# Kernel tuning notes

Hardware: AMD Instinct MI355X
Metric: run time of the kernel (lower is better)

Reference implementation:

```python
import jax, jax.numpy as jnp
import numpy as np

B, T, E = 2, 2048, 1024
H = 16
DH = E // H  # 64
DFF = 4 * E
EPS = 1e-5


def _layernorm(x, gamma, beta):
    mu = jnp.mean(x, axis=-1, keepdims=True)
    var = jnp.mean((x - mu) ** 2, axis=-1, keepdims=True)
    return (x - mu) * jax.lax.rsqrt(var + EPS) * gamma + beta


def setup_inputs() -> dict:
    key = jax.random.key(0)
    ks = jax.random.split(key, 16)
    s_e = 1.0 / np.sqrt(E)
    s_f = 1.0 / np.sqrt(DFF)
    return {
        "x": jax.random.normal(ks[0], (B, T, E), jnp.float32),
        # per-head QKV projections, stacked over heads [H, E, DH]
        "Wq": jax.random.normal(ks[1], (H, E, DH), jnp.float32) * s_e,
        "bq": jnp.zeros((H, DH), jnp.float32),
        "Wk": jax.random.normal(ks[2], (H, E, DH), jnp.float32) * s_e,
        "bk": jnp.zeros((H, DH), jnp.float32),
        "Wv": jax.random.normal(ks[3], (H, E, DH), jnp.float32) * s_e,
        "bv": jnp.zeros((H, DH), jnp.float32),
        # output projection
        "Wo": jax.random.normal(ks[4], (E, E), jnp.float32) * s_e,
        "bo": jnp.zeros((E,), jnp.float32),
        # feed-forward
        "W1": jax.random.normal(ks[5], (E, DFF), jnp.float32) * s_e,
        "b1": jnp.zeros((DFF,), jnp.float32),
        "W2": jax.random.normal(ks[6], (DFF, E), jnp.float32) * s_f,
        "b2": jnp.zeros((E,), jnp.float32),
        # layernorms
        "gamma1": jnp.ones((E,), jnp.float32),
        "beta1": jnp.zeros((E,), jnp.float32),
        "gamma2": jnp.ones((E,), jnp.float32),
        "beta2": jnp.zeros((E,), jnp.float32),
    }


def reference(x, Wq, bq, Wk, bk, Wv, bv, Wo, bo, W1, b1, W2, b2,
              gamma1, beta1, gamma2, beta2):
    Bc, Tc, Ec = x.shape
    # --- multi-head causal self-attention (dropout = eval/identity) ---
    xn = _layernorm(x, gamma1, beta1)
    q = jnp.einsum('bte,hed->bhtd', xn, Wq) + bq[:, None, :]
    k = jnp.einsum('bte,hed->bhtd', xn, Wk) + bk[:, None, :]
    v = jnp.einsum('bte,hed->bhtd', xn, Wv) + bv[:, None, :]
    scale = 1.0 / np.sqrt(q.shape[-1])
    scores = jnp.einsum('bhtd,bhsd->bhts', q, k) * scale  # [B,H,T,T]
    causal = jnp.tril(jnp.ones((Tc, Tc), bool))
    scores = jnp.where(causal, scores, jnp.float32(-1e9))
    attn = jax.nn.softmax(scores, axis=-1)
    out = jnp.einsum('bhts,bhsd->bhtd', attn, v)          # [B,H,T,DH]
    out = out.transpose(0, 2, 1, 3).reshape(Bc, Tc, Ec)    # concat heads
    out = out @ Wo + bo
    x = x + out
    # --- feed-forward ---
    xn2 = _layernorm(x, gamma2, beta2)
    h = jax.nn.relu(xn2 @ W1 + b1)
    x = x + (h @ W2 + b2)
    return x
```

## Files before the change

kernel.cpp:

```cpp
#include <hip/hip_runtime.h>
#include <stdint.h>

#define BT    4096
#define EDIM  1024
#define TLEN  2048
#define NH    16
#define DHH   64
#define DFFN  4096

typedef short short8 __attribute__((ext_vector_type(8)));
typedef float f32x4  __attribute__((ext_vector_type(4)));

typedef const __attribute__((address_space(1))) unsigned int* gas_ptr;
typedef __attribute__((address_space(3))) unsigned int*       las_ptr;

__device__ __forceinline__ float bf2f(unsigned short u) {
    union { unsigned int i; float f; } c; c.i = ((unsigned int)u) << 16; return c.f;
}
__device__ __forceinline__ unsigned short f2bf(float f) {
    union { float f; unsigned int i; } c; c.f = f;
    unsigned int u = c.i;
    unsigned int r = u + 0x7fffu + ((u >> 16) & 1u);
    return (unsigned short)(r >> 16);
}
__device__ __forceinline__ unsigned short f2bf_trunc(float f) {
    union { float f; unsigned int i; } c; c.f = f;
    return (unsigned short)(c.i >> 16);
}
__device__ __forceinline__ float fexp2(float x) {
#if __has_builtin(__builtin_amdgcn_exp2f)
    return __builtin_amdgcn_exp2f(x);
#else
    return __expf(x * 0.69314718056f);
#endif
}
__device__ __forceinline__ void gload16(const unsigned short* g, unsigned short* l) {
    __builtin_amdgcn_global_load_lds((gas_ptr)g, (las_ptr)l, 16, 0, 0);
}

template<int QKV>
__global__ __launch_bounds__(256) void transpose_kernel(
    const float* src, unsigned short* dst, int Kdim, int srcStride)
{
    __shared__ float T[64][65];
    int t = threadIdx.x;
    int n0 = blockIdx.x * 64, k0 = blockIdx.y * 64;
    int r = t >> 4, c4 = (t & 15) * 4;
    #pragma unroll
    for (int i = 0; i < 4; i++) {
        int rr = r + i * 16;
        const float* p;
        if (QKV) p = src + ((size_t)(n0 >> 6)) * 65536 + (size_t)(k0 + rr) * 64 + c4;
        else     p = src + (size_t)(k0 + rr) * srcStride + n0 + c4;
        float4 v = *(const float4*)p;
        T[c4 + 0][rr] = v.x;
        T[c4 + 1][rr] = v.y;
        T[c4 + 2][rr] = v.z;
        T[c4 + 3][rr] = v.w;
    }
    __syncthreads();
    int rn = t >> 2, ck = (t & 3) * 16;
    short8 o0, o1;
    #pragma unroll
    for (int j = 0; j < 8; j++) o0[j] = (short)f2bf(T[rn][ck + j]);
    #pragma unroll
    for (int j = 0; j < 8; j++) o1[j] = (short)f2bf(T[rn][ck + 8 + j]);
    unsigned short* dp = dst + (size_t)(n0 + rn) * Kdim + k0 + ck;
    *(short8*)dp       = o0;
    *(short8*)(dp + 8) = o1;
}

__global__ __launch_bounds__(256) void transpose_qkv3_kernel(
    const float* __restrict__ Wq, const float* __restrict__ Wk,
    const float* __restrict__ Wv, unsigned short* __restrict__ dstbase)
{
    __shared__ float T[64][65];
    int z = blockIdx.z;
    const float* src = (z == 0) ? Wq : (z == 1) ? Wk : Wv;
    unsigned short* dst = dstbase + (size_t)z * 1048576;
    int t = threadIdx.x;
    int n0 = blockIdx.x * 64, k0 = blockIdx.y * 64;
    int r = t >> 4, c4 = (t & 15) * 4;
    #pragma unroll
    for (int i = 0; i < 4; i++) {
        int rr = r + i * 16;
        const float* p = src + ((size_t)(n0 >> 6)) * 65536 + (size_t)(k0 + rr) * 64 + c4;
        float4 v = *(const float4*)p;
        T[c4 + 0][rr] = v.x;
        T[c4 + 1][rr] = v.y;
        T[c4 + 2][rr] = v.z;
        T[c4 + 3][rr] = v.w;
    }
    __syncthreads();
    int rn = t >> 2, ck = (t & 3) * 16;
    short8 o0, o1;
    #pragma unroll
    for (int j = 0; j < 8; j++) o0[j] = (short)f2bf(T[rn][ck + j]);
    #pragma unroll
    for (int j = 0; j < 8; j++) o1[j] = (short)f2bf(T[rn][ck + 8 + j]);
    unsigned short* dp = dst + (size_t)(n0 + rn) * EDIM + k0 + ck;
    *(short8*)dp       = o0;
    *(short8*)(dp + 8) = o1;
}

__global__ __launch_bounds__(256) void vtrans_kernel(
    const unsigned short* __restrict__ v, unsigned short* __restrict__ vt)
{
    __shared__ __align__(16) unsigned short T[64][72];
    int bh = blockIdx.x, st = blockIdx.y;
    int t = threadIdx.x;
    int r = t >> 2, c = (t & 3) * 16;
    const unsigned short* src = v + ((size_t)bh * TLEN + st * 64) * DHH;
    short8 a0 = *(const short8*)(src + r * DHH + c);
    short8 a1 = *(const short8*)(src + r * DHH + c + 8);
    *(short8*)&T[r][c]     = a0;
    *(short8*)&T[r][c + 8] = a1;
    __syncthreads();
    int d = t >> 2;
    short8 o0, o1;
    #pragma unroll
    for (int j = 0; j < 8; j++) o0[j] = (short)T[c + j][d];
    #pragma unroll
    for (int j = 0; j < 8; j++) o1[j] = (short)T[c + 8 + j][d];
    unsigned short* dst = vt + ((size_t)bh * DHH + d) * TLEN + st * 64 + c;
    *(short8*)dst       = o0;
    *(short8*)(dst + 8) = o1;
}

__global__ __launch_bounds__(256) void bias_fuse_kernel(
    const float* __restrict__ bq, const float* __restrict__ bk,
    const float* __restrict__ bv, float* __restrict__ dst)
{
    int t = blockIdx.x * 256 + threadIdx.x;
    const float* src = (t < 1024) ? bq : (t < 2048) ? bk : bv;
    dst[t] = src[t & 1023];
}

template<int F32IN>
__global__ __launch_bounds__(256) void ln_fused_kernel(
    const void* __restrict__ x, const float* __restrict__ g,
    const float* __restrict__ b, unsigned short* __restrict__ out)
{
    int row = blockIdx.x, tid = threadIdx.x;
    size_t off = (size_t)row * EDIM + tid * 4;
    float v0, v1, v2, v3;
    if (F32IN) {
        float4 a = *(const float4*)((const float*)x + off);
        v0 = a.x; v1 = a.y; v2 = a.z; v3 = a.w;
    } else {
        ushort4 raw = *(const ushort4*)((const unsigned short*)x + off);
        v0 = bf2f(raw.x); v1 = bf2f(raw.y); v2 = bf2f(raw.z); v3 = bf2f(raw.w);
    }
    float s  = v0 + v1 + v2 + v3;
    float ss = v0*v0 + v1*v1 + v2*v2 + v3*v3;
    #pragma unroll
    for (int o = 1; o < 64; o <<= 1) {
        s  += __shfl_xor(s,  o, 64);
        ss += __shfl_xor(ss, o, 64);
    }
    __shared__ float red[8];
    int wave = tid >> 6;
    if ((tid & 63) == 0) { red[wave*2] = s; red[wave*2+1] = ss; }
    __syncthreads();
    s  = red[0] + red[2] + red[4] + red[6];
    ss = red[1] + red[3] + red[5] + red[7];
    float m  = s * (1.0f / EDIM);
    float rs = rsqrtf(ss * (1.0f / EDIM) - m * m + 1e-5f);
    float4 gv = *(const float4*)(g + tid * 4);
    float4 bv = *(const float4*)(b + tid * 4);
    ushort4 o;
    o.x = f2bf((v0 - m) * rs * gv.x + bv.x);
    o.y = f2bf((v1 - m) * rs * gv.y + bv.y);
    o.z = f2bf((v2 - m) * rs * gv.z + bv.z);
    o.w = f2bf((v3 - m) * rs * gv.w + bv.w);
    *(ushort4*)(out + off) = o;
}

#define V_QKV  0
#define V_WO   1
#define V_FF1  2
#define V_FF2A 3
#define V_FF2B 4

template<int VARIANT, int BN>
__global__ __launch_bounds__(256) void gemm_bt_kernel(
    const unsigned short* A,
    const unsigned short* Bt,
    const float* bias,
    const void* resid,
    void* out,
    int N, int K)
{
    constexpr int NJ = BN / 32;
    __shared__ __align__(16) unsigned short As[128 * 64];
    __shared__ __align__(16) unsigned short Bs[BN * 64];
    int tid  = threadIdx.x;
    int lane = tid & 63, wave = tid >> 6;
    int quad = lane >> 4, l16 = lane & 15;
    int wr = wave >> 1, wc = wave & 1;
    int m0 = blockIdx.y * 128, n0 = blockIdx.x * BN;

    f32x4 acc[4][NJ];
    #pragma unroll
    for (int i = 0; i < 4; i++)
        #pragma unroll
        for (int j = 0; j < NJ; j++) acc[i][j] = (f32x4){0.f, 0.f, 0.f, 0.f};

    int lr = lane >> 3;
    int lc = (lane & 7) * 8;

    for (int k0 = 0; k0 < K; k0 += 64) {
        #pragma unroll
        for (int i = 0; i < 4; i++) {
            int r = (i * 4 + wave) * 8 + lr;
            gload16(A + (size_t)(m0 + r) * K + k0 + lc, &As[(i * 4 + wave) * 512]);
        }
        #pragma unroll
        for (int i = 0; i < NJ; i++) {
            int r = (i * 4 + wave) * 8 + lr;
            gload16(Bt + (size_t)(n0 + r) * K + k0 + lc, &Bs[(i * 4 + wave) * 512]);
        }
        __syncthreads();

        #pragma unroll
        for (int ks = 0; ks < 2; ks++) {
            short8 af[4], bf[NJ];
            #pragma unroll
            for (int i = 0; i < 4; i++)
                af[i] = *(const short8*)(&As[(wr * 64 + i * 16 + l16) * 64 + ks * 32 + quad * 8]);
            #pragma unroll
            for (int j = 0; j < NJ; j++)
                bf[j] = *(const short8*)(&Bs[(wc * (BN / 2) + j * 16 + l16) * 64 + ks * 32 + quad * 8]);
            #pragma unroll
            for (int i = 0; i < 4; i++)
                #pragma unroll
                for (int j = 0; j < NJ; j++)
                    acc[i][j] = __builtin_amdgcn_mfma_f32_16x16x32_bf16(af[i], bf[j], acc[i][j], 0, 0, 0);
        }

        __syncthreads();
    }

    #pragma unroll
    for (int j = 0; j < NJ; j++) {
        int c = n0 + wc * (BN / 2) + j * 16 + l16;
        float bi = (VARIANT == V_FF2A) ? 0.0f : bias[c];
        #pragma unroll
        for (int i = 0; i < 4; i++) {
            #pragma unroll
            for (int r = 0; r < 4; r++) {
                int m = m0 + wr * 64 + i * 16 + quad * 4 + r;
                float val = acc[i][j][r] + bi;
                if (VARIANT == V_WO)
                    val += ((const float*)resid)[(size_t)m * N + c];
                if (VARIANT == V_FF2B)
                    val += bf2f(((const unsigned short*)resid)[(size_t)m * N + c])
                         + ((const float*)out)[(size_t)m * N + c];
                if (VARIANT == V_FF1)
                    val = fmaxf(val, 0.0f);
                if (VARIANT == V_QKV) {
                    int b = m >> 11, t = m & 2047;
                    int mat = c >> 10, cc = c & 1023;
                    int h = cc >> 6, d = cc & 63;
                    ((unsigned short*)out)[(size_t)mat * 4194304 +
                        (((size_t)(b * NH + h)) * TLEN + t) * DHH + d] = f2bf(val);
                } else if (VARIANT == V_FF2A || VARIANT == V_FF2B) {
                    ((float*)out)[(size_t)m * N + c] = val;
                } else {
                    ((unsigned short*)out)[(size_t)m * N + c] = f2bf(val);
                }
            }
        }
    }
}

__global__ __launch_bounds__(256) void attn_kernel(
    const unsigned short* __restrict__ q,
    const unsigned short* __restrict__ k,
    const unsigned short* __restrict__ vt,
    unsigned short* __restrict__ att)
{
    __shared__ __align__(16) unsigned short Ks[128 * 72];
    __shared__ __align__(16) unsigned short Vs[64 * 136];
    __shared__ __align__(16) unsigned short Ps[4][16 * 136];
    int tid  = threadIdx.x;
    int lane = tid & 63, wave = tid >> 6;
    int quad = lane >> 4, l16 = lane & 15;

    int flat = blockIdx.x;
    int xcd  = flat & 7, idx = flat >> 3;
    int bh   = xcd * 4 + (idx >> 5);
    int qt   = 31 - (idx & 31);
    int q0   = qt * 64;
    int qw   = q0 + wave * 16;

    const unsigned short* Qb = q  + ((size_t)bh * TLEN + qw) * DHH;
    const unsigned short* Kb = k  + (size_t)bh * TLEN * DHH;
    const unsigned short* Vb = vt + (size_t)bh * DHH * TLEN;

    short8 aq0 = *(const short8*)(Qb + l16 * DHH + quad * 8);
    short8 aq1 = *(const short8*)(Qb + l16 * DHH + 32 + quad * 8);

    f32x4 o[4];
    #pragma unroll
    for (int n = 0; n < 4; n++) o[n] = (f32x4){0.f, 0.f, 0.f, 0.f};
    f32x4 mrow = {-1e30f, -1e30f, -1e30f, -1e30f};
    f32x4 lrow = {0.f, 0.f, 0.f, 0.f};
    unsigned short* Pw = Ps[wave];
    const float cs = 0.18033688011f;

    int rowK = tid >> 1, colK = (tid & 1) * 32;
    int rowV = tid >> 2, colV = (tid & 3) * 32;

    int nch = (q0 >> 7) + 1;

    short8 ka0, ka1, ka2, ka3, va0, va1, va2, va3;
    {
        const unsigned short* kp = Kb + (size_t)rowK * DHH + colK;
        ka0 = *(const short8*)kp;
        ka1 = *(const short8*)(kp + 8);
        ka2 = *(const short8*)(kp + 16);
        ka3 = *(const short8*)(kp + 24);
        const unsigned short* vp = Vb + (size_t)rowV * TLEN + colV;
        va0 = *(const short8*)vp;
        va1 = *(const short8*)(vp + 8);
        va2 = *(const short8*)(vp + 16);
        va3 = *(const short8*)(vp + 24);
    }

    for (int ch = 0; ch < nch; ch++) {
        int s0 = ch * 128;
        __syncthreads();
        *(short8*)(&Ks[rowK * 72 + colK])       = ka0;
        *(short8*)(&Ks[rowK * 72 + colK + 8])   = ka1;
        *(short8*)(&Ks[rowK * 72 + colK + 16])  = ka2;
        *(short8*)(&Ks[rowK * 72 + colK + 24])  = ka3;
        *(short8*)(&Vs[rowV * 136 + colV])      = va0;
        *(short8*)(&Vs[rowV * 136 + colV + 8])  = va1;
        *(short8*)(&Vs[rowV * 136 + colV + 16]) = va2;
        *(short8*)(&Vs[rowV * 136 + colV + 24]) = va3;
        __syncthreads();

        if (ch + 1 < nch) {
            int s1 = s0 + 128;
            const unsigned short* kp = Kb + (size_t)(s1 + rowK) * DHH + colK;
            ka0 = *(const short8*)kp;
            ka1 = *(const short8*)(kp + 8);
            ka2 = *(const short8*)(kp + 16);
            ka3 = *(const short8*)(kp + 24);
            const unsigned short* vp = Vb + (size_t)rowV * TLEN + s1 + colV;
            va0 = *(const short8*)vp;
            va1 = *(const short8*)(vp + 8);
            va2 = *(const short8*)(vp + 16);
            va3 = *(const short8*)(vp + 24);
        }

        f32x4 S[8];
        #pragma unroll
        for (int n = 0; n < 8; n++) {
            short8 b0 = *(const short8*)(&Ks[(n * 16 + l16) * 72 + quad * 8]);
            short8 b1 = *(const short8*)(&Ks[(n * 16 + l16) * 72 + 32 + quad * 8]);
            f32x4 s = (f32x4){0.f, 0.f, 0.f, 0.f};
            s = __builtin_amdgcn_mfma_f32_16x16x32_bf16(aq0, b0, s, 0, 0, 0);
            s = __builtin_amdgcn_mfma_f32_16x16x32_bf16(aq1, b1, s, 0, 0, 0);
            S[n] = s;
        }
        bool needmask = (s0 + 127 > qw);
        #pragma unroll
        for (int r = 0; r < 4; r++) {
            float xv[8];
            #pragma unroll
            for (int n = 0; n < 8; n++) {
                float xx = S[n][r] * cs;
                if (needmask && (s0 + n * 16 + l16 > qw + quad * 4 + r)) xx = -1e30f;
                xv[n] = xx;
            }
            float mxl = fmaxf(fmaxf(fmaxf(xv[0], xv[1]), fmaxf(xv[2], xv[3])),
                              fmaxf(fmaxf(xv[4], xv[5]), fmaxf(xv[6], xv[7])));
            float used;
            if (__all(mxl <= mrow[r] + 8.0f)) {
                used = mrow[r];
            } else {
                float mx = mxl;
                mx = fmaxf(mx, __shfl_xor(mx, 1, 64));
                mx = fmaxf(mx, __shfl_xor(mx, 2, 64));
                mx = fmaxf(mx, __shfl_xor(mx, 4, 64));
                mx = fmaxf(mx, __shfl_xor(mx, 8, 64));
                float mnew  = fmaxf(mrow[r], mx);
                float alpha = fexp2(mrow[r] - mnew);
                lrow[r] *= alpha;
                o[0][r] *= alpha; o[1][r] *= alpha;
                o[2][r] *= alpha; o[3][r] *= alpha;
                mrow[r] = mnew;
                used = mnew;
            }
            float ps = 0.f;
            int prow = (quad * 4 + r) * 136;
            #pragma unroll
            for (int n = 0; n < 8; n++) {
                float p = fexp2(xv[n] - used);
                ps += p;
                Pw[prow + n * 16 + l16] = f2bf_trunc(p);
            }
            lrow[r] += ps;
        }
        short8 ap[4];
        #pragma unroll
        for (int ks = 0; ks < 4; ks++)
            ap[ks] = *(const short8*)(Pw + l16 * 136 + ks * 32 + quad * 8);
        #pragma unroll
        for (int n = 0; n < 4; n++) {
            #pragma unroll
            for (int ks = 0; ks < 4; ks++) {
                short8 b = *(const short8*)(&Vs[(n * 16 + l16) * 136 + ks * 32 + quad * 8]);
                o[n] = __builtin_amdgcn_mfma_f32_16x16x32_bf16(ap[ks], b, o[n], 0, 0, 0);
            }
        }
    }

    int bidx = bh >> 4, hh = bh & 15;
    #pragma unroll
    for (int r = 0; r < 4; r++) {
        float ls = lrow[r];
        ls += __shfl_xor(ls, 1, 64);
        ls += __shfl_xor(ls, 2, 64);
        ls += __shfl_xor(ls, 4, 64);
        ls += __shfl_xor(ls, 8, 64);
        float inv = 1.0f / ls;
        int t = qw + quad * 4 + r;
        size_t rowoff = ((size_t)(bidx * TLEN + t)) * EDIM + hh * 64;
        #pragma unroll
        for (int n = 0; n < 4; n++)
            att[rowoff + n * 16 + l16] = f2bf(o[n][r] * inv);
    }
}

extern "C" void kernel_launch(void* const* d_in, const int* in_sizes, int n_in,
                              void* d_out, int out_size, void* d_ws, size_t ws_size,
                              hipStream_t stream)
{
    (void)in_sizes; (void)n_in; (void)out_size; (void)ws_size;
    const float* x   = (const float*)d_in[0];
    const float* Wq  = (const float*)d_in[1];
    const float* bq  = (const float*)d_in[2];
    const float* Wk  = (const float*)d_in[3];
    const float* bk  = (const float*)d_in[4];
    const float* Wv  = (const float*)d_in[5];
    const float* bv  = (const float*)d_in[6];
    const float* Wo  = (const float*)d_in[7];
    const float* bo  = (const float*)d_in[8];
    const float* W1  = (const float*)d_in[9];
    const float* b1  = (const float*)d_in[10];
    const float* W2  = (const float*)d_in[11];
    const float* b2  = (const float*)d_in[12];
    const float* g1  = (const float*)d_in[13];
    const float* be1 = (const float*)d_in[14];
    const float* g2  = (const float*)d_in[15];
    const float* be2 = (const float*)d_in[16];

    unsigned short* ws  = (unsigned short*)d_ws;
    unsigned short* xn  = ws;
    unsigned short* vtg = ws;
    unsigned short* qb  = ws + 4194304;
    unsigned short* kb  = ws + 8388608;
    unsigned short* vb  = ws + 12582912;
    unsigned short* wqt = ws + 16777216;
    unsigned short* att = ws + 16777216;
    unsigned short* x1  = ws + 4194304;
    unsigned short* wot = ws + 8388608;
    unsigned short* w1t = ws + 8388608;
    unsigned short* w2t = ws + 10485760;
    unsigned short* hb  = ws + 12582912;
    float* biasf = (float*)(ws + 19922944);

    dim3 gT64(16, 16);
    dim3 gE(EDIM / 64, BT / 128);
    dim3 gQKV(3072 / 128, BT / 128);
    dim3 gF(2048 / 128, BT / 128);

    transpose_qkv3_kernel<<<dim3(16, 16, 3), 256, 0, stream>>>(Wq, Wk, Wv, wqt);
    bias_fuse_kernel<<<dim3(12), 256, 0, stream>>>(bq, bk, bv, biasf);

    ln_fused_kernel<1><<<BT, 256, 0, stream>>>(x, g1, be1, xn);

    gemm_bt_kernel<V_QKV, 128><<<gQKV, 256, 0, stream>>>(xn, wqt, biasf, nullptr, qb, 3072, EDIM);

    vtrans_kernel<<<dim3(NH * 2, TLEN / 64), 256, 0, stream>>>(vb, vtg);

    attn_kernel<<<dim3(1024), 256, 0, stream>>>(qb, kb, vtg, att);

    transpose_kernel<0><<<gT64, 256, 0, stream>>>(Wo, wot, EDIM, EDIM);
    gemm_bt_kernel<V_WO, 64><<<gE, 256, 0, stream>>>(att, wot, bo, x, x1, EDIM, EDIM);

    ln_fused_kernel<0><<<BT, 256, 0, stream>>>(x1, g2, be2, xn);

    transpose_kernel<0><<<dim3(32, 16), 256, 0, stream>>>(W1, w1t, EDIM, DFFN);
    transpose_kernel<0><<<dim3(16, 32), 256, 0, stream>>>(W2, w2t, 2048, EDIM);
    gemm_bt_kernel<V_FF1, 128><<<gF, 256, 0, stream>>>(xn, w1t, b1, nullptr, hb, 2048, EDIM);
    gemm_bt_kernel<V_FF2A, 64><<<gE, 256, 0, stream>>>(hb, w2t, nullptr, nullptr, d_out, EDIM, 2048);
    transpose_kernel<0><<<dim3(32, 16), 256, 0, stream>>>(W1 + 2048, w1t, EDIM, DFFN);
    transpose_kernel<0><<<dim3(16, 32), 256, 0, stream>>>(W2 + (size_t)2048 * EDIM, w2t, 2048, EDIM);
    gemm_bt_kernel<V_FF1, 128><<<gF, 256, 0, stream>>>(xn, w1t, b1 + 2048, nullptr, hb, 2048, EDIM);
    gemm_bt_kernel<V_FF2B, 64><<<gE, 256, 0, stream>>>(hb, w2t, b2, x1, d_out, EDIM, 2048);
}
```

Before: 442.5 us.

## Process two query tiles per attention block, swizzle GEMM grid, fuse FFN transposes

The attention kernel now handles 128 query rows per block, with each wave processing two 16-row groups, so every K/V chunk loaded into shared memory serves twice as many queries and the block count halves. The GEMMs switch to a 1D grid with an XCD-aware remap of block index to tile, intended to improve L2 locality across the chiplets. The paired W1/W2 transpose launches are merged into a single kernel using blockIdx.z, which cuts launch count. Costs are higher register pressure in attention and fewer blocks, which may worsen causal load imbalance.

```diff
diff --git a/kernel.cpp b/kernel.cpp
--- a/kernel.cpp
+++ b/kernel.cpp
@@ -99,6 +99,43 @@
     #pragma unroll
     for (int j = 0; j < 8; j++) o1[j] = (short)f2bf(T[rn][ck + 8 + j]);
     unsigned short* dp = dst + (size_t)(n0 + rn) * EDIM + k0 + ck;
+    *(short8*)dp       = o0;
+    *(short8*)(dp + 8) = o1;
+}
+
+__global__ __launch_bounds__(256) void transpose_ffn_kernel(
+    const float* __restrict__ W1h, const float* __restrict__ W2h,
+    unsigned short* __restrict__ w1t, unsigned short* __restrict__ w2t)
+{
+    __shared__ float T[64][65];
+    int z = blockIdx.z;
+    const float* src;
+    unsigned short* dst;
+    int Kdim, sstride, n0, k0;
+    if (z == 0) { src = W1h; dst = w1t; Kdim = 1024; sstride = 4096;
+                  n0 = blockIdx.x * 64; k0 = blockIdx.y * 64; }
+    else        { src = W2h; dst = w2t; Kdim = 2048; sstride = 1024;
+                  n0 = blockIdx.y * 64; k0 = blockIdx.x * 64; }
+    int t = threadIdx.x;
+    int r = t >> 4, c4 = (t & 15) * 4;
+    #pragma unroll
+    for (int i = 0; i < 4; i++) {
+        int rr = r + i * 16;
+        const float* p = src + (size_t)(k0 + rr) * sstride + n0 + c4;
+        float4 v = *(const float4*)p;
+        T[c4 + 0][rr] = v.x;
+        T[c4 + 1][rr] = v.y;
+        T[c4 + 2][rr] = v.z;
+        T[c4 + 3][rr] = v.w;
+    }
+    __syncthreads();
+    int rn = t >> 2, ck = (t & 3) * 16;
+    short8 o0, o1;
+    #pragma unroll
+    for (int j = 0; j < 8; j++) o0[j] = (short)f2bf(T[rn][ck + j]);
+    #pragma unroll
+    for (int j = 0; j < 8; j++) o1[j] = (short)f2bf(T[rn][ck + 8 + j]);
+    unsigned short* dp = dst + (size_t)(n0 + rn) * Kdim + k0 + ck;
     *(short8*)dp       = o0;
     *(short8*)(dp + 8) = o1;
 }
@@ -189,7 +226,7 @@
     const float* bias,
     const void* resid,
     void* out,
-    int N, int K)
+    int N, int K, int gx)
 {
     constexpr int NJ = BN / 32;
     __shared__ __align__(16) unsigned short As[128 * 64];
@@ -198,7 +235,11 @@
     int lane = tid & 63, wave = tid >> 6;
     int quad = lane >> 4, l16 = lane & 15;
     int wr = wave >> 1, wc = wave & 1;
-    int m0 = blockIdx.y * 128, n0 = blockIdx.x * BN;
+
+    int cpx  = (int)gridDim.x >> 3;
+    int flat = blockIdx.x;
+    int wg   = (flat & 7) * cpx + (flat >> 3);
+    int m0 = (wg / gx) * 128, n0 = (wg % gx) * BN;
 
     f32x4 acc[4][NJ];
     #pragma unroll
@@ -274,6 +315,76 @@
     }
 }
 
+__device__ __forceinline__ void attn_qh_pass(
+    const short8& aqa, const short8& aqb,
+    const unsigned short* Ks, const unsigned short* Vs, unsigned short* Pw,
+    f32x4* o, f32x4& mrow, f32x4& lrow,
+    int s0, int qw, int quad, int l16)
+{
+    const float cs = 0.18033688011f;
+    f32x4 S[8];
+    #pragma unroll
+    for (int n = 0; n < 8; n++) {
+        short8 b0 = *(const short8*)(&Ks[(n * 16 + l16) * 72 + quad * 8]);
+        short8 b1 = *(const short8*)(&Ks[(n * 16 + l16) * 72 + 32 + quad * 8]);
+        f32x4 s = (f32x4){0.f, 0.f, 0.f, 0.f};
+        s = __builtin_amdgcn_mfma_f32_16x16x32_bf16(aqa, b0, s, 0, 0, 0);
+        s = __builtin_amdgcn_mfma_f32_16x16x32_bf16(aqb, b1, s, 0, 0, 0);
+        S[n] = s;
+    }
+    bool needmask = (s0 + 127 > qw);
+    #pragma unroll
+    for (int r = 0; r < 4; r++) {
+        float xv[8];
+        #pragma unroll
+        for (int n = 0; n < 8; n++) {
+            float xx = S[n][r] * cs;
+            if (needmask && (s0 + n * 16 + l16 > qw + quad * 4 + r)) xx = -1e30f;
+            xv[n] = xx;
+        }
+        float mxl = fmaxf(fmaxf(fmaxf(xv[0], xv[1]), fmaxf(xv[2], xv[3])),
+                          fmaxf(fmaxf(xv[4], xv[5]), fmaxf(xv[6], xv[7])));
+        float used;
+        if (__all(mxl <= mrow[r] + 8.0f)) {
+            used = mrow[r];
+        } else {
+            float mx = mxl;
+            mx = fmaxf(mx, __shfl_xor(mx, 1, 64));
+            mx = fmaxf(mx, __shfl_xor(mx, 2, 64));
+            mx = fmaxf(mx, __shfl_xor(mx, 4, 64));
+            mx = fmaxf(mx, __shfl_xor(mx, 8, 64));
+            float mnew  = fmaxf(mrow[r], mx);
+            float alpha = fexp2(mrow[r] - mnew);
+            lrow[r] *= alpha;
+            o[0][r] *= alpha; o[1][r] *= alpha;
+            o[2][r] *= alpha; o[3][r] *= alpha;
+            mrow[r] = mnew;
+            used = mnew;
+        }
+        float ps = 0.f;
+        int prow = (quad * 4 + r) * 136;
+        #pragma unroll
+        for (int n = 0; n < 8; n++) {
+            float p = fexp2(xv[n] - used);
+            ps += p;
+            Pw[prow + n * 16 + l16] = f2bf_trunc(p);
+        }
+        lrow[r] += ps;
+    }
+    short8 ap[4];
+    #pragma unroll
+    for (int ks = 0; ks < 4; ks++)
+        ap[ks] = *(const short8*)(Pw + l16 * 136 + ks * 32 + quad * 8);
+    #pragma unroll
+    for (int n = 0; n < 4; n++) {
+        #pragma unroll
+        for (int ks = 0; ks < 4; ks++) {
+            short8 b = *(const short8*)(&Vs[(n * 16 + l16) * 136 + ks * 32 + quad * 8]);
+            o[n] = __builtin_amdgcn_mfma_f32_16x16x32_bf16(ap[ks], b, o[n], 0, 0, 0);
+        }
+    }
+}
+
 __global__ __launch_bounds__(256) void attn_kernel(
     const unsigned short* __restrict__ q,
     const unsigned short* __restrict__ k,
@@ -289,30 +400,36 @@
 
     int flat = blockIdx.x;
     int xcd  = flat & 7, idx = flat >> 3;
-    int bh   = xcd * 4 + (idx >> 5);
-    int qt   = 31 - (idx & 31);
-    int q0   = qt * 64;
-    int qw   = q0 + wave * 16;
-
-    const unsigned short* Qb = q  + ((size_t)bh * TLEN + qw) * DHH;
+    int bh   = xcd * 4 + (idx >> 4);
+    int qt   = 15 - (idx & 15);
+    int q0   = qt * 128;
+    int qw0  = q0 + wave * 16;
+    int qw1  = qw0 + 64;
+
     const unsigned short* Kb = k  + (size_t)bh * TLEN * DHH;
     const unsigned short* Vb = vt + (size_t)bh * DHH * TLEN;
-
-    short8 aq0 = *(const short8*)(Qb + l16 * DHH + quad * 8);
-    short8 aq1 = *(const short8*)(Qb + l16 * DHH + 32 + quad * 8);
-
-    f32x4 o[4];
-    #pragma unroll
-    for (int n = 0; n < 4; n++) o[n] = (f32x4){0.f, 0.f, 0.f, 0.f};
-    f32x4 mrow = {-1e30f, -1e30f, -1e30f, -1e30f};
-    f32x4 lrow = {0.f, 0.f, 0.f, 0.f};
+    const unsigned short* Q0 = q + ((size_t)bh * TLEN + qw0) * DHH;
+    const unsigned short* Q1 = q + ((size_t)bh * TLEN + qw1) * DHH;
+
+    short8 aq00 = *(const short8*)(Q0 + l16 * DHH + quad * 8);
+    short8 aq01 = *(const short8*)(Q0 + l16 * DHH + 32 + quad * 8);
+    short8 aq10 = *(const short8*)(Q1 + l16 * DHH + quad * 8);
+    short8 aq11 = *(const short8*)(Q1 + l16 * DHH + 32 + quad * 8);
+
+    f32x4 o0[4], o1[4];
+    #pragma unroll
+    for (int n = 0; n < 4; n++) {
+        o0[n] = (f32x4){0.f, 0.f, 0.f, 0.f};
+        o1[n] = (f32x4){0.f, 0.f, 0.f, 0.f};
+    }
+    f32x4 mrow0 = {-1e30f, -1e30f, -1e30f, -1e30f}, mrow1 = mrow0;
+    f32x4 lrow0 = {0.f, 0.f, 0.f, 0.f},            lrow1 = lrow0;
     unsigned short* Pw = Ps[wave];
-    const float cs = 0.18033688011f;
 
     int rowK = tid >> 1, colK = (tid & 1) * 32;
     int rowV = tid >> 2, colV = (tid & 3) * 32;
 
-    int nch = (q0 >> 7) + 1;
+    int nch = qt + 1;
 
     short8 ka0, ka1, ka2, ka3, va0, va1, va2, va3;
     {
@@ -355,83 +472,38 @@
             va3 = *(const short8*)(vp + 24);
         }
 
-        f32x4 S[8];
-        #pragma unroll
-        for (int n = 0; n < 8; n++) {
-            short8 b0 = *(const short8*)(&Ks[(n * 16 + l16) * 72 + quad * 8]);
-            short8 b1 = *(const short8*)(&Ks[(n * 16 + l16) * 72 + 32 + quad * 8]);
-            f32x4 s = (f32x4){0.f, 0.f, 0.f, 0.f};
-            s = __builtin_amdgcn_mfma_f32_16x16x32_bf16(aq0, b0, s, 0, 0, 0);
-            s = __builtin_amdgcn_mfma_f32_16x16x32_bf16(aq1, b1, s, 0, 0, 0);
-            S[n] = s;
-        }
-        bool needmask = (s0 + 127 > qw);
-        #pragma unroll
-        for (int r = 0; r < 4; r++) {
-            float xv[8];
-            #pragma unroll
-            for (int n = 0; n < 8; n++) {
-                float xx = S[n][r] * cs;
-                if (needmask && (s0 + n * 16 + l16 > qw + quad * 4 + r)) xx = -1e30f;
-                xv[n] = xx;
-            }
-            float mxl = fmaxf(fmaxf(fmaxf(xv[0], xv[1]), fmaxf(xv[2], xv[3])),
-                              fmaxf(fmaxf(xv[4], xv[5]), fmaxf(xv[6], xv[7])));
-            float used;
-            if (__all(mxl <= mrow[r] + 8.0f)) {
-                used = mrow[r];
-            } else {
-                float mx = mxl;
-                mx = fmaxf(mx, __shfl_xor(mx, 1, 64));
-                mx = fmaxf(mx, __shfl_xor(mx, 2, 64));
-                mx = fmaxf(mx, __shfl_xor(mx, 4, 64));
-                mx = fmaxf(mx, __shfl_xor(mx, 8, 64));
-                float mnew  = fmaxf(mrow[r], mx);
-                float alpha = fexp2(mrow[r] - mnew);
-                lrow[r] *= alpha;
-                o[0][r] *= alpha; o[1][r] *= alpha;
-                o[2][r] *= alpha; o[3][r] *= alpha;
-                mrow[r] = mnew;
-                used = mnew;
-            }
-            float ps = 0.f;
-            int prow = (quad * 4 + r) * 136;
-            #pragma unroll
-            for (int n = 0; n < 8; n++) {
-                float p = fexp2(xv[n] - used);
-                ps += p;
-                Pw[prow + n * 16 + l16] = f2bf_trunc(p);
-            }
-            lrow[r] += ps;
-        }
-        short8 ap[4];
-        #pragma unroll
-        for (int ks = 0; ks < 4; ks++)
-            ap[ks] = *(const short8*)(Pw + l16 * 136 + ks * 32 + quad * 8);
-        #pragma unroll
-        for (int n = 0; n < 4; n++) {
-            #pragma unroll
-            for (int ks = 0; ks < 4; ks++) {
-                short8 b = *(const short8*)(&Vs[(n * 16 + l16) * 136 + ks * 32 + quad * 8]);
-                o[n] = __builtin_amdgcn_mfma_f32_16x16x32_bf16(ap[ks], b, o[n], 0, 0, 0);
-            }
-        }
+        attn_qh_pass(aq00, aq01, Ks, Vs, Pw, o0, mrow0, lrow0, s0, qw0, quad, l16);
+        attn_qh_pass(aq10, aq11, Ks, Vs, Pw, o1, mrow1, lrow1, s0, qw1, quad, l16);
     }
 
     int bidx = bh >> 4, hh = bh & 15;
     #pragma unroll
     for (int r = 0; r < 4; r++) {
-        float ls = lrow[r];
+        float ls = lrow0[r];
         ls += __shfl_xor(ls, 1, 64);
         ls += __shfl_xor(ls, 2, 64);
         ls += __shfl_xor(ls, 4, 64);
         ls += __shfl_xor(ls, 8, 64);
         float inv = 1.0f / ls;
-        int t = qw + quad * 4 + r;
+        int t = qw0 + quad * 4 + r;
         size_t rowoff = ((size_t)(bidx * TLEN + t)) * EDIM + hh * 64;
         #pragma unroll
         for (int n = 0; n < 4; n++)
-            att[rowoff + n * 16 + l16] = f2bf(o[n][r] * inv);
+            att[rowoff + n * 16 + l16] = f2bf(o0[n][r] * inv);
+    }
+    #pragma unroll
+    for (int r = 0; r < 4; r++) {
+        float ls = lrow1[r];
+        ls += __shfl_xor(ls, 1, 64);
+        ls += __shfl_xor(ls, 2, 64);
+        ls += __shfl_xor(ls, 4, 64);
+        ls += __shfl_xor(ls, 8, 64);
+        float inv = 1.0f / ls;
+        int t = qw1 + quad * 4 + r;
+        size_t rowoff = ((size_t)(bidx * TLEN + t)) * EDIM + hh * 64;
+        #pragma unroll
+        for (int n = 0; n < 4; n++)
+            att[rowoff + n * 16 + l16] = f2bf(o1[n][r] * inv);
     }
 }
 
@@ -474,32 +546,27 @@
     float* biasf = (float*)(ws + 19922944);
 
     dim3 gT64(16, 16);
-    dim3 gE(EDIM / 64, BT / 128);
-    dim3 gQKV(3072 / 128, BT / 128);
-    dim3 gF(2048 / 128, BT / 128);
 
     transpose_qkv3_kernel<<<dim3(16, 16, 3), 256, 0, stream>>>(Wq, Wk, Wv, wqt);
     bias_fuse_kernel<<<dim3(12), 256, 0, stream>>>(bq, bk, bv, biasf);
 
     ln_fused_kernel<1><<<BT, 256, 0, stream>>>(x, g1, be1, xn);
 
-    gemm_bt_kernel<V_QKV, 128><<<gQKV, 256, 0, stream>>>(xn, wqt, biasf, nullptr, qb, 3072, EDIM);
+    gemm_bt_kernel<V_QKV, 128><<<768, 256, 0, stream>>>(xn, wqt, biasf, nullptr, qb, 3072, EDIM, 24);
 
     vtrans_kernel<<<dim3(NH * 2, TLEN / 64), 256, 0, stream>>>(vb, vtg);
 
-    attn_kernel<<<dim3(1024), 256, 0, stream>>>(qb, kb, vtg, att);
+    attn_kernel<<<dim3(512), 256, 0, stream>>>(qb, kb, vtg, att);
 
     transpose_kernel<0><<<gT64, 256, 0, stream>>>(Wo, wot, EDIM, EDIM);
-    gemm_bt_kernel<V_WO, 64><<<gE, 256, 0, stream>>>(att, wot, bo, x, x1, EDIM, EDIM);
+    gemm_bt_kernel<V_WO, 64><<<512, 256, 0, stream>>>(att, wot, bo, x, x1, EDIM, EDIM, 16);
 
     ln_fused_kernel<0><<<BT, 256, 0, stream>>>(x1, g2, be2, xn);
 
-    transpose_kernel<0><<<dim3(32, 16), 256, 0, stream>>>(W1, w1t, EDIM, DFFN);
-    transpose_kernel<0><<<dim3(16, 32), 256, 0, stream>>>(W2, w2t, 2048, EDIM);
-    gemm_bt_kernel<V_FF1, 128><<<gF, 256, 0, stream>>>(xn, w1t, b1, nullptr, hb, 2048, EDIM);
-    gemm_bt_kernel<V_FF2A, 64><<<gE, 256, 0, stream>>>(hb, w2t, nullptr, nullptr, d_out, EDIM, 2048);
-    transpose_kernel<0><<<dim3(32, 16), 256, 0, stream>>>(W1 + 2048, w1t, EDIM, DFFN);
-    transpose_kernel<0><<<dim3(16, 32), 256, 0, stream>>>(W2 + (size_t)2048 * EDIM, w2t, 2048, EDIM);
-    gemm_bt_kernel<V_FF1, 128><<<gF, 256, 0, stream>>>(xn, w1t, b1 + 2048, nullptr, hb, 2048, EDIM);
-    gemm_bt_kernel<V_FF2B, 64><<<gE, 256, 0, stream>>>(hb, w2t, b2, x1, d_out, EDIM, 2048);
-}
+    transpose_ffn_kernel<<<dim3(32, 16, 2), 256, 0, stream>>>(W1, W2, w1t, w2t);
+    gemm_bt_kernel<V_FF1, 128><<<512, 256, 0, stream>>>(xn, w1t, b1, nullptr, hb, 2048, EDIM, 16);
+    gemm_bt_kernel<V_FF2A, 64><<<512, 256, 0, stream>>>(hb, w2t, nullptr, nullptr, d_out, EDIM, 2048, 16);
+    transpose_ffn_kernel<<<dim3(32, 16, 2), 256, 0, stream>>>(W1 + 2048, W2 + (size_t)2048 * EDIM, w1t, w2t);
+    gemm_bt_kernel<V_FF1, 128><<<512, 256, 0, stream>>>(xn, w1t, b1 + 2048, nullptr, hb, 2048, EDIM, 16);
+    gemm_bt_kernel<V_FF2B, 64><<<512, 256, 0, stream>>>(hb, w2t, b2, x1, d_out, EDIM, 2048, 16);
+}
```

Result: slower. 470.7 us (+6.4%).
